# Performance work log

Measured on AMD Instinct MI355X. Metric: run time of the kernel, lower is better.

The kernel has to match this reference:

```python
import jax, jax.numpy as jnp
import numpy as np

N, D = 8192, 128

def setup_inputs() -> dict:
    key = jax.random.key(0)
    kq, kk, kv = jax.random.split(key, 3)
    return {
        "query": jax.random.normal(kq, (N, D), dtype=jnp.float32),
        "key": jax.random.normal(kk, (N, D), dtype=jnp.float32),
        "value": jax.random.normal(kv, (N, D), dtype=jnp.float32),
    }

def reference(query, key, value):
    # FlashAttentionV1 computes exact (non-causal, unmasked) softmax attention:
    # softmax(Q K^T / sqrt(d)) V, via tiled online softmax. The math is
    # identical to the dense formulation below.
    d = query.shape[-1]
    scores = jnp.einsum('qd,kd->qk', query, key) / jnp.sqrt(jnp.asarray(d, query.dtype))
    probs = jax.nn.softmax(scores, axis=-1)
    return jnp.einsum('qk,kd->qd', probs, value)
```

## Files before the change

kernel.cpp:

```cpp
#include <hip/hip_runtime.h>

#define NTOK 8192
#define DH   128
#define QBLK 128
#define KVB  64
#define TILES (NTOK / KVB)

typedef __attribute__((ext_vector_type(8)))  short bf16x8;
typedef __attribute__((ext_vector_type(16))) float f32x16;
typedef __attribute__((ext_vector_type(4)))  unsigned short u16x4;

typedef __attribute__((address_space(1))) const void gv_t;
typedef __attribute__((address_space(3))) void sv_t;

static __device__ __forceinline__ unsigned short f2bf(float x) {
  union { float f; unsigned int u; } a; a.f = x;
  unsigned int r = a.u + 0x7FFFu + ((a.u >> 16) & 1u);
  return (unsigned short)(r >> 16);
}

static __device__ __forceinline__ unsigned pk2(float lo, float hi) {
  unsigned r;
  asm("v_cvt_pk_bf16_f32 %0, %1, %2" : "=v"(r) : "v"(lo), "v"(hi));
  return r;
}

static __device__ __forceinline__ f32x16 zero16() {
  f32x16 v;
  #pragma unroll
  for (int i = 0; i < 16; ++i) v[i] = 0.f;
  return v;
}

__global__ __launch_bounds__(256)
void fa_prep(const float* __restrict__ Kg, const float* __restrict__ Vg,
             char* __restrict__ Kimg, char* __restrict__ Vimg)
{
  const int t = blockIdx.x;
  const int tid = threadIdx.x;

  {
    const int krow = tid >> 2;
    const int kcg  = (tid & 3) * 32;
    const float* src = Kg + ((size_t)t * KVB + krow) * DH + kcg;
    char* drow = Kimg + (size_t)t * 16384 + krow * 256;
    const int sw = (krow & 15) << 4;
    #pragma unroll
    for (int w = 0; w < 4; ++w) {
      float4 a = *reinterpret_cast<const float4*>(src + w * 8);
      float4 b = *reinterpret_cast<const float4*>(src + w * 8 + 4);
      union { bf16x8 v; unsigned short u[8]; } f;
      f.u[0] = f2bf(a.x); f.u[1] = f2bf(a.y); f.u[2] = f2bf(a.z); f.u[3] = f2bf(a.w);
      f.u[4] = f2bf(b.x); f.u[5] = f2bf(b.y); f.u[6] = f2bf(b.z); f.u[7] = f2bf(b.w);
      *reinterpret_cast<bf16x8*>(drow + ((kcg * 2 + w * 16) ^ sw)) = f.v;
    }
  }

  {
    #pragma unroll
    for (int it = 0; it < 2; ++it) {
      int task = tid + it * 256;
      int kvl  = (task & 15) * 4;
      int d0   = (task >> 4) * 4;
      const float* src = Vg + ((size_t)t * KVB + kvl) * DH + d0;
      float4 r0 = *reinterpret_cast<const float4*>(src);
      float4 r1 = *reinterpret_cast<const float4*>(src + DH);
      float4 r2 = *reinterpret_cast<const float4*>(src + 2 * DH);
      float4 r3 = *reinterpret_cast<const float4*>(src + 3 * DH);
      char* base = Vimg + (size_t)t * 16384;
      const int bb = kvl * 2;
      { int d = d0 + 0;
        u16x4 w4 = (u16x4){f2bf(r0.x), f2bf(r1.x), f2bf(r2.x), f2bf(r3.x)};
        *reinterpret_cast<u16x4*>(base + d * 128 + (bb ^ ((d & 15) << 3))) = w4; }
      { int d = d0 + 1;
        u16x4 w4 = (u16x4){f2bf(r0.y), f2bf(r1.y), f2bf(r2.y), f2bf(r3.y)};
        *reinterpret_cast<u16x4*>(base + d * 128 + (bb ^ ((d & 15) << 3))) = w4; }
      { int d = d0 + 2;
        u16x4 w4 = (u16x4){f2bf(r0.z), f2bf(r1.z), f2bf(r2.z), f2bf(r3.z)};
        *reinterpret_cast<u16x4*>(base + d * 128 + (bb ^ ((d & 15) << 3))) = w4; }
      { int d = d0 + 3;
        u16x4 w4 = (u16x4){f2bf(r0.w), f2bf(r1.w), f2bf(r2.w), f2bf(r3.w)};
        *reinterpret_cast<u16x4*>(base + d * 128 + (bb ^ ((d & 15) << 3))) = w4; }
    }
  }
}

static __device__ __forceinline__ void softmax_half(
    const f32x16& st, float& m_run, float& l_run, f32x16* oacc,
    bf16x8& pfa, bf16x8& pfb)
{
  float a0 = fmaxf(st[0],  st[1]),  a1 = fmaxf(st[2],  st[3]);
  float a2 = fmaxf(st[4],  st[5]),  a3 = fmaxf(st[6],  st[7]);
  float a4 = fmaxf(st[8],  st[9]),  a5 = fmaxf(st[10], st[11]);
  float a6 = fmaxf(st[12], st[13]), a7 = fmaxf(st[14], st[15]);
  float b0 = fmaxf(a0, a1), b1 = fmaxf(a2, a3);
  float b2 = fmaxf(a4, a5), b3 = fmaxf(a6, a7);
  float pmax = fmaxf(fmaxf(b0, b1), fmaxf(b2, b3));
  if (!__all(pmax <= m_run + 8.f)) {
    pmax = fmaxf(pmax, __shfl_xor(pmax, 32));
    const float m_new = fmaxf(m_run, pmax);
    const float corr  = (m_run > -1e30f) ? exp2f(m_run - m_new) : 0.f;
    l_run *= corr;
    #pragma unroll
    for (int i = 0; i < 4; ++i) oacc[i] = oacc[i] * corr;
    m_run = m_new;
  }
  float e[16];
  #pragma unroll
  for (int r = 0; r < 16; ++r) e[r] = exp2f(st[r] - m_run);
  float s0 = (e[0] + e[1])   + (e[2] + e[3]);
  float s1 = (e[4] + e[5])   + (e[6] + e[7]);
  float s2 = (e[8] + e[9])   + (e[10] + e[11]);
  float s3 = (e[12] + e[13]) + (e[14] + e[15]);
  l_run += (s0 + s1) + (s2 + s3);
  union { bf16x8 v; unsigned u[4]; } fa, fb;
  fa.u[0] = pk2(e[0],  e[1]);  fa.u[1] = pk2(e[2],  e[3]);
  fa.u[2] = pk2(e[4],  e[5]);  fa.u[3] = pk2(e[6],  e[7]);
  fb.u[0] = pk2(e[8],  e[9]);  fb.u[1] = pk2(e[10], e[11]);
  fb.u[2] = pk2(e[12], e[13]); fb.u[3] = pk2(e[14], e[15]);
  pfa = fa.v; pfb = fb.v;
}

__global__ __launch_bounds__(256, 3)
void fa_fwd(const float* __restrict__ Qg, const char* __restrict__ Kimg,
            const char* __restrict__ Vimg, float* __restrict__ Od,
            float* __restrict__ Mp, float* __restrict__ Lp, int ksplit)
{
  __shared__ __align__(16) char smem[49152];
  const int tid  = threadIdx.x;
  const int lane = tid & 63;
  const int wv   = tid >> 6;
  const int l31  = lane & 31;
  const int hi   = lane >> 5;

  const int q0blk = blockIdx.x * QBLK;
  const int q     = q0blk + wv * 32 + l31;
  const int chunk = blockIdx.y;
  const float QSCALE = 0.1275313310087464f;

  const int bt    = TILES / ksplit;
  const int rem   = TILES - bt * ksplit;
  const int tile0 = chunk * bt + (chunk < rem ? chunk : rem);
  const int nst   = bt + (chunk < rem ? 1 : 0);

  bf16x8 qf[8];
  {
    const float* qs = Qg + (size_t)q * DH + hi * 8;
    #pragma unroll
    for (int kc = 0; kc < 8; ++kc) {
      float4 a = *reinterpret_cast<const float4*>(qs + kc * 16);
      float4 b = *reinterpret_cast<const float4*>(qs + kc * 16 + 4);
      union { bf16x8 v; unsigned u[4]; } f;
      f.u[0] = pk2(a.x * QSCALE, a.y * QSCALE);
      f.u[1] = pk2(a.z * QSCALE, a.w * QSCALE);
      f.u[2] = pk2(b.x * QSCALE, b.y * QSCALE);
      f.u[3] = pk2(b.z * QSCALE, b.w * QSCALE);
      qf[kc] = f.v;
    }
  }

  const char* gbase = (wv < 2 ? Kimg : Vimg);
  const size_t goff = (size_t)(wv & 1) * 8192 + (size_t)lane * 16;
  const int    lK   = (wv & 1) * 8192;
  const int    lV   = 32768 + (wv & 1) * 8192;

#define STAGE_K(B, T) do { if (wv < 2) {                                      \
    const char* _s = gbase + (size_t)(T) * 16384 + goff;                      \
    char* _d = &smem[(B) * 16384 + lK];                                       \
    _Pragma("unroll")                                                         \
    for (int _i = 0; _i < 8; ++_i)                                            \
      __builtin_amdgcn_global_load_lds((gv_t*)(_s + _i * 1024),               \
                                       (sv_t*)(_d + _i * 1024), 16, 0, 0);    \
  } } while (0)

#define STAGE_V(T) do { if (wv >= 2) {                                        \
    const char* _s = gbase + (size_t)(T) * 16384 + goff;                      \
    char* _d = &smem[lV];                                                     \
    _Pragma("unroll")                                                         \
    for (int _i = 0; _i < 8; ++_i)                                            \
      __builtin_amdgcn_global_load_lds((gv_t*)(_s + _i * 1024),               \
                                       (sv_t*)(_d + _i * 1024), 16, 0, 0);    \
  } } while (0)

  STAGE_K(0, tile0);
  STAGE_K(1, tile0 + 1);
  STAGE_V(tile0);

  f32x16 oacc[4];
  #pragma unroll
  for (int i = 0; i < 4; ++i) oacc[i] = zero16();
  float m_run = -INFINITY, l_run = 0.f;

  int cur = 0;
  for (int t = 0; t < nst; ++t) {
    if (wv < 2) {
      if (t + 1 < nst) asm volatile("s_waitcnt vmcnt(8)" ::: "memory");
      else             asm volatile("s_waitcnt vmcnt(0)" ::: "memory");
    }
    __builtin_amdgcn_sched_barrier(0);
    __builtin_amdgcn_s_barrier();

    const char* smK = &smem[cur * 16384];
    const char* smV = &smem[32768];
    const int swk = (l31 & 15) << 4;
    const int swv = (l31 & 15) << 3;

    f32x16 st0 = zero16(), st1 = zero16();
    __builtin_amdgcn_s_setprio(1);
    #pragma unroll
    for (int kc = 0; kc < 8; ++kc) {
      const int cb = (kc * 32 + hi * 16) ^ swk;
      bf16x8 a0 = *reinterpret_cast<const bf16x8*>(smK + l31 * 256 + cb);
      st0 = __builtin_amdgcn_mfma_f32_32x32x16_bf16(a0, qf[kc], st0, 0, 0, 0);
      bf16x8 a1 = *reinterpret_cast<const bf16x8*>(smK + (l31 + 32) * 256 + cb);
      st1 = __builtin_amdgcn_mfma_f32_32x32x16_bf16(a1, qf[kc], st1, 0, 0, 0);
    }
    __builtin_amdgcn_s_setprio(0);

    bf16x8 pf0a, pf0b, pf1a, pf1b;
    softmax_half(st0, m_run, l_run, oacc, pf0a, pf0b);
    softmax_half(st1, m_run, l_run, oacc, pf1a, pf1b);

    if (wv >= 2) asm volatile("s_waitcnt vmcnt(0)" ::: "memory");
    __builtin_amdgcn_sched_barrier(0);
    __builtin_amdgcn_s_barrier();

    __builtin_amdgcn_s_setprio(1);
    #pragma unroll
    for (int c = 0; c < 4; ++c) {
      const bf16x8 pb = (c == 0) ? pf0a : (c == 1) ? pf0b : (c == 2) ? pf1a : pf1b;
      #pragma unroll
      for (int dt = 0; dt < 4; ++dt) {
        const char* vb = smV + (dt * 32 + l31) * 128;
        union { bf16x8 v; u16x4 h[2]; } a;
        a.h[0] = *reinterpret_cast<const u16x4*>(vb + ((c * 32 + 8 * hi) ^ swv));
        a.h[1] = *reinterpret_cast<const u16x4*>(vb + ((c * 32 + 16 + 8 * hi) ^ swv));
        oacc[dt] = __builtin_amdgcn_mfma_f32_32x32x16_bf16(a.v, pb, oacc[dt], 0, 0, 0);
      }
    }
    __builtin_amdgcn_s_setprio(0);

    __builtin_amdgcn_s_barrier();
    if (t + 2 < nst) STAGE_K(cur, tile0 + t + 2);
    if (t + 1 < nst) STAGE_V(tile0 + t + 1);
    cur ^= 1;
  }
#undef STAGE_K
#undef STAGE_V

  const float l_tot = l_run + __shfl_xor(l_run, 32);
  const float scale = (ksplit == 1) ? (1.f / l_tot) : 1.f;
  float* dstB = (ksplit == 1) ? Od : Od + (size_t)chunk * NTOK * DH;

  char* base = &smem[(wv & 1) * 16384];
  const int qloc4 = lane >> 2;
  const int s4    = lane & 3;
  #pragma unroll
  for (int ph = 0; ph < 2; ++ph) {
    __builtin_amdgcn_s_barrier();
    if ((wv >> 1) == ph) {
      #pragma unroll
      for (int dt = 0; dt < 4; ++dt)
        #pragma unroll
        for (int rg = 0; rg < 4; ++rg)
          #pragma unroll
          for (int j = 0; j < 4; ++j) {
            const int d = dt * 32 + rg * 8 + hi * 4 + j;
            *reinterpret_cast<float*>(base + d * 128 + l31 * 4) =
                oacc[dt][rg * 4 + j] * scale;
          }
      asm volatile("s_waitcnt lgkmcnt(0)" ::: "memory");
      __builtin_amdgcn_sched_barrier(0);
      #pragma unroll
      for (int qh = 0; qh < 2; ++qh) {
        const int qloc = qh * 16 + qloc4;
        float* dst = dstB + (size_t)(q0blk + wv * 32 + qloc) * DH;
        #pragma unroll
        for (int i = 0; i < 8; ++i) {
          const int dd = s4 * 4 + i * 16;
          float4 v;
          v.x = *reinterpret_cast<float*>(base + (dd + 0) * 128 + qloc * 4);
          v.y = *reinterpret_cast<float*>(base + (dd + 1) * 128 + qloc * 4);
          v.z = *reinterpret_cast<float*>(base + (dd + 2) * 128 + qloc * 4);
          v.w = *reinterpret_cast<float*>(base + (dd + 3) * 128 + qloc * 4);
          *reinterpret_cast<float4*>(dst + dd) = v;
        }
      }
    }
  }

  if (ksplit > 1 && lane < 32) {
    const int qg = q0blk + wv * 32 + lane;
    Mp[chunk * NTOK + qg] = m_run;
    Lp[chunk * NTOK + qg] = l_tot;
  }
}

__global__ __launch_bounds__(256)
void fa_combine(const float* __restrict__ Op, const float* __restrict__ Mp,
                const float* __restrict__ Lp, float* __restrict__ out, int ksplit)
{
  const int gid = blockIdx.x * 256 + threadIdx.x;
  const int q   = gid >> 5;
  const int dv  = (gid & 31) * 4;
  float mx = -INFINITY;
  for (int c = 0; c < ksplit; ++c) mx = fmaxf(mx, Mp[c * NTOK + q]);
  float den = 0.f;
  float ax = 0.f, ay = 0.f, az = 0.f, aw = 0.f;
  for (int c = 0; c < ksplit; ++c) {
    const float w = exp2f(Mp[c * NTOK + q] - mx);
    den += w * Lp[c * NTOK + q];
    float4 o = *reinterpret_cast<const float4*>(Op + (size_t)c * NTOK * DH + (size_t)q * DH + dv);
    ax += w * o.x; ay += w * o.y; az += w * o.z; aw += w * o.w;
  }
  const float r = 1.f / den;
  float4 res; res.x = ax * r; res.y = ay * r; res.z = az * r; res.w = aw * r;
  *reinterpret_cast<float4*>(out + (size_t)q * DH + dv) = res;
}

extern "C" void kernel_launch(void* const* d_in, const int* in_sizes, int n_in,
                              void* d_out, int out_size, void* d_ws, size_t ws_size,
                              hipStream_t stream)
{
  const float* Q = (const float*)d_in[0];
  const float* K = (const float*)d_in[1];
  const float* V = (const float*)d_in[2];
  float* out = (float*)d_out;

  auto need = [](size_t ks) {
    return ks * (size_t)NTOK * DH * 4 + 2 * ks * (size_t)NTOK * 4;
  };
  int KS = (ws_size >= need(12)) ? 12 : 8;

  char* Kimg = (char*)d_out;
  char* Vimg = Kimg + (size_t)NTOK * 256;

  float* Op = (float*)d_ws;
  float* Mp = Op + (size_t)KS * NTOK * DH;
  float* Lp = Mp + (size_t)KS * NTOK;

  fa_prep<<<TILES, 256, 0, stream>>>(K, V, Kimg, Vimg);
  fa_fwd<<<dim3(NTOK / QBLK, KS), 256, 0, stream>>>(Q, Kimg, Vimg, Op, Mp, Lp, KS);
  fa_combine<<<NTOK * DH / 4 / 256, 256, 0, stream>>>(Op, Mp, Lp, out, KS);
}
```

Before: 73.92 us.

## Software-pipeline QK^T of next tile with PV MFMAs using double-buffered V

Restructures the main attention loop so the QK^T MFMAs for the next KV tile are interleaved with the PV MFMAs of the current tile, and softmax runs on scores computed in the previous iteration. V is now double-buffered in 64KB LDS and K/V prefetches are issued right after softmax. The split count drops from 12 to 8 (or fewer) with occupancy hint lowered to 2 blocks, and the epilogue writes all four waves at once without phasing. This aims to hide softmax and load latency behind matrix work, at the cost of more registers, more LDS and fewer resident blocks.

```diff
diff --git a/kernel.cpp b/kernel.cpp
--- a/kernel.cpp
+++ b/kernel.cpp
@@ -4,7 +4,6 @@
 #define DH   128
 #define QBLK 128
 #define KVB  64
-#define TILES (NTOK / KVB)
 
 typedef __attribute__((ext_vector_type(8)))  short bf16x8;
 typedef __attribute__((ext_vector_type(16))) float f32x16;
@@ -121,12 +120,13 @@
   pfa = fa.v; pfb = fb.v;
 }
 
-__global__ __launch_bounds__(256, 3)
+__global__ __launch_bounds__(256, 2)
 void fa_fwd(const float* __restrict__ Qg, const char* __restrict__ Kimg,
             const char* __restrict__ Vimg, float* __restrict__ Od,
-            float* __restrict__ Mp, float* __restrict__ Lp, int ksplit)
-{
-  __shared__ __align__(16) char smem[49152];
+            float* __restrict__ Mp, float* __restrict__ Lp,
+            int ksplit, int chunk_len)
+{
+  __shared__ __align__(16) char smem[65536];
   const int tid  = threadIdx.x;
   const int lane = tid & 63;
   const int wv   = tid >> 6;
@@ -138,10 +138,8 @@
   const int chunk = blockIdx.y;
   const float QSCALE = 0.1275313310087464f;
 
-  const int bt    = TILES / ksplit;
-  const int rem   = TILES - bt * ksplit;
-  const int tile0 = chunk * bt + (chunk < rem ? chunk : rem);
-  const int nst   = bt + (chunk < rem ? 1 : 0);
+  const int tile0 = (chunk * chunk_len) >> 6;
+  const int nst   = chunk_len >> 6;
 
   bf16x8 qf[8];
   {
@@ -161,21 +159,20 @@
 
   const char* gbase = (wv < 2 ? Kimg : Vimg);
   const size_t goff = (size_t)(wv & 1) * 8192 + (size_t)lane * 16;
-  const int    lK   = (wv & 1) * 8192;
-  const int    lV   = 32768 + (wv & 1) * 8192;
+  const int    lofs = (wv & 1) * 8192;
 
 #define STAGE_K(B, T) do { if (wv < 2) {                                      \
     const char* _s = gbase + (size_t)(T) * 16384 + goff;                      \
-    char* _d = &smem[(B) * 16384 + lK];                                       \
+    char* _d = &smem[(B) * 16384 + lofs];                                     \
     _Pragma("unroll")                                                         \
     for (int _i = 0; _i < 8; ++_i)                                            \
       __builtin_amdgcn_global_load_lds((gv_t*)(_s + _i * 1024),               \
                                        (sv_t*)(_d + _i * 1024), 16, 0, 0);    \
   } } while (0)
 
-#define STAGE_V(T) do { if (wv >= 2) {                                        \
+#define STAGE_V(B, T) do { if (wv >= 2) {                                     \
     const char* _s = gbase + (size_t)(T) * 16384 + goff;                      \
-    char* _d = &smem[lV];                                                     \
+    char* _d = &smem[32768 + (B) * 16384 + lofs];                             \
     _Pragma("unroll")                                                         \
     for (int _i = 0; _i < 8; ++_i)                                            \
       __builtin_amdgcn_global_load_lds((gv_t*)(_s + _i * 1024),               \
@@ -184,29 +181,22 @@
 
   STAGE_K(0, tile0);
   STAGE_K(1, tile0 + 1);
-  STAGE_V(tile0);
+  STAGE_V(0, tile0);
 
   f32x16 oacc[4];
   #pragma unroll
   for (int i = 0; i < 4; ++i) oacc[i] = zero16();
   float m_run = -INFINITY, l_run = 0.f;
-
-  int cur = 0;
-  for (int t = 0; t < nst; ++t) {
-    if (wv < 2) {
-      if (t + 1 < nst) asm volatile("s_waitcnt vmcnt(8)" ::: "memory");
-      else             asm volatile("s_waitcnt vmcnt(0)" ::: "memory");
-    }
-    __builtin_amdgcn_sched_barrier(0);
-    __builtin_amdgcn_s_barrier();
-
-    const char* smK = &smem[cur * 16384];
-    const char* smV = &smem[32768];
-    const int swk = (l31 & 15) << 4;
-    const int swv = (l31 & 15) << 3;
-
-    f32x16 st0 = zero16(), st1 = zero16();
-    __builtin_amdgcn_s_setprio(1);
+  const int swk = (l31 & 15) << 4;
+  const int swv = (l31 & 15) << 3;
+
+  if (wv < 2) asm volatile("s_waitcnt vmcnt(8)" ::: "memory");
+  __builtin_amdgcn_sched_barrier(0);
+  __builtin_amdgcn_s_barrier();
+
+  f32x16 st0 = zero16(), st1 = zero16();
+  {
+    const char* smK = &smem[0];
     #pragma unroll
     for (int kc = 0; kc < 8; ++kc) {
       const int cb = (kc * 32 + hi * 16) ^ swk;
@@ -215,35 +205,59 @@
       bf16x8 a1 = *reinterpret_cast<const bf16x8*>(smK + (l31 + 32) * 256 + cb);
       st1 = __builtin_amdgcn_mfma_f32_32x32x16_bf16(a1, qf[kc], st1, 0, 0, 0);
     }
-    __builtin_amdgcn_s_setprio(0);
-
+  }
+  __builtin_amdgcn_s_barrier();
+
+  for (int t = 0; t < nst; ++t) {
     bf16x8 pf0a, pf0b, pf1a, pf1b;
     softmax_half(st0, m_run, l_run, oacc, pf0a, pf0b);
     softmax_half(st1, m_run, l_run, oacc, pf1a, pf1b);
 
-    if (wv >= 2) asm volatile("s_waitcnt vmcnt(0)" ::: "memory");
+    if (t + 2 < nst) STAGE_K(t & 1, tile0 + t + 2);
+    if (t + 1 < nst) STAGE_V((t + 1) & 1, tile0 + t + 1);
+
+    if (wv < 2) {
+      if (t + 2 < nst) asm volatile("s_waitcnt vmcnt(8)" ::: "memory");
+      else             asm volatile("s_waitcnt vmcnt(0)" ::: "memory");
+    } else {
+      if (t + 1 < nst) asm volatile("s_waitcnt vmcnt(8)" ::: "memory");
+      else             asm volatile("s_waitcnt vmcnt(0)" ::: "memory");
+    }
     __builtin_amdgcn_sched_barrier(0);
     __builtin_amdgcn_s_barrier();
 
+    const char* smK = &smem[((t + 1) & 1) * 16384];
+    const char* smV = &smem[32768 + (t & 1) * 16384];
+    const bool doqk = (t + 1 < nst);
+    f32x16 ns0 = zero16(), ns1 = zero16();
     __builtin_amdgcn_s_setprio(1);
     #pragma unroll
-    for (int c = 0; c < 4; ++c) {
-      const bf16x8 pb = (c == 0) ? pf0a : (c == 1) ? pf0b : (c == 2) ? pf1a : pf1b;
+    for (int g = 0; g < 4; ++g) {
+      if (doqk) {
+        #pragma unroll
+        for (int kk = 0; kk < 2; ++kk) {
+          const int kc = g * 2 + kk;
+          const int cb = (kc * 32 + hi * 16) ^ swk;
+          bf16x8 a0 = *reinterpret_cast<const bf16x8*>(smK + l31 * 256 + cb);
+          ns0 = __builtin_amdgcn_mfma_f32_32x32x16_bf16(a0, qf[kc], ns0, 0, 0, 0);
+          bf16x8 a1 = *reinterpret_cast<const bf16x8*>(smK + (l31 + 32) * 256 + cb);
+          ns1 = __builtin_amdgcn_mfma_f32_32x32x16_bf16(a1, qf[kc], ns1, 0, 0, 0);
+        }
+      }
+      const bf16x8 pb = (g == 0) ? pf0a : (g == 1) ? pf0b : (g == 2) ? pf1a : pf1b;
       #pragma unroll
       for (int dt = 0; dt < 4; ++dt) {
         const char* vb = smV + (dt * 32 + l31) * 128;
         union { bf16x8 v; u16x4 h[2]; } a;
-        a.h[0] = *reinterpret_cast<const u16x4*>(vb + ((c * 32 + 8 * hi) ^ swv));
-        a.h[1] = *reinterpret_cast<const u16x4*>(vb + ((c * 32 + 16 + 8 * hi) ^ swv));
+        a.h[0] = *reinterpret_cast<const u16x4*>(vb + ((g * 32 + 8 * hi) ^ swv));
+        a.h[1] = *reinterpret_cast<const u16x4*>(vb + ((g * 32 + 16 + 8 * hi) ^ swv));
         oacc[dt] = __builtin_amdgcn_mfma_f32_32x32x16_bf16(a.v, pb, oacc[dt], 0, 0, 0);
       }
     }
     __builtin_amdgcn_s_setprio(0);
+    st0 = ns0; st1 = ns1;
 
     __builtin_amdgcn_s_barrier();
-    if (t + 2 < nst) STAGE_K(cur, tile0 + t + 2);
-    if (t + 1 < nst) STAGE_V(tile0 + t + 1);
-    cur ^= 1;
   }
 #undef STAGE_K
 #undef STAGE_V
@@ -252,40 +266,34 @@
   const float scale = (ksplit == 1) ? (1.f / l_tot) : 1.f;
   float* dstB = (ksplit == 1) ? Od : Od + (size_t)chunk * NTOK * DH;
 
-  char* base = &smem[(wv & 1) * 16384];
+  char* base = &smem[0] + wv * 16384;
+  #pragma unroll
+  for (int dt = 0; dt < 4; ++dt)
+    #pragma unroll
+    for (int rg = 0; rg < 4; ++rg)
+      #pragma unroll
+      for (int j = 0; j < 4; ++j) {
+        const int d = dt * 32 + rg * 8 + hi * 4 + j;
+        *reinterpret_cast<float*>(base + d * 128 + l31 * 4) =
+            oacc[dt][rg * 4 + j] * scale;
+      }
+  asm volatile("s_waitcnt lgkmcnt(0)" ::: "memory");
+  __builtin_amdgcn_sched_barrier(0);
   const int qloc4 = lane >> 2;
   const int s4    = lane & 3;
   #pragma unroll
-  for (int ph = 0; ph < 2; ++ph) {
-    __builtin_amdgcn_s_barrier();
-    if ((wv >> 1) == ph) {
-      #pragma unroll
-      for (int dt = 0; dt < 4; ++dt)
-        #pragma unroll
-        for (int rg = 0; rg < 4; ++rg)
-          #pragma unroll
-          for (int j = 0; j < 4; ++j) {
-            const int d = dt * 32 + rg * 8 + hi * 4 + j;
-            *reinterpret_cast<float*>(base + d * 128 + l31 * 4) =
-                oacc[dt][rg * 4 + j] * scale;
-          }
-      asm volatile("s_waitcnt lgkmcnt(0)" ::: "memory");
-      __builtin_amdgcn_sched_barrier(0);
-      #pragma unroll
-      for (int qh = 0; qh < 2; ++qh) {
-        const int qloc = qh * 16 + qloc4;
-        float* dst = dstB + (size_t)(q0blk + wv * 32 + qloc) * DH;
-        #pragma unroll
-        for (int i = 0; i < 8; ++i) {
-          const int dd = s4 * 4 + i * 16;
-          float4 v;
-          v.x = *reinterpret_cast<float*>(base + (dd + 0) * 128 + qloc * 4);
-          v.y = *reinterpret_cast<float*>(base + (dd + 1) * 128 + qloc * 4);
-          v.z = *reinterpret_cast<float*>(base + (dd + 2) * 128 + qloc * 4);
-          v.w = *reinterpret_cast<float*>(base + (dd + 3) * 128 + qloc * 4);
-          *reinterpret_cast<float4*>(dst + dd) = v;
-        }
-      }
+  for (int qh = 0; qh < 2; ++qh) {
+    const int qloc = qh * 16 + qloc4;
+    float* dst = dstB + (size_t)(q0blk + wv * 32 + qloc) * DH;
+    #pragma unroll
+    for (int i = 0; i < 8; ++i) {
+      const int dd = s4 * 4 + i * 16;
+      float4 v;
+      v.x = *reinterpret_cast<float*>(base + (dd + 0) * 128 + qloc * 4);
+      v.y = *reinterpret_cast<float*>(base + (dd + 1) * 128 + qloc * 4);
+      v.z = *reinterpret_cast<float*>(base + (dd + 2) * 128 + qloc * 4);
+      v.w = *reinterpret_cast<float*>(base + (dd + 3) * 128 + qloc * 4);
+      *reinterpret_cast<float4*>(dst + dd) = v;
     }
   }
 
@@ -330,7 +338,7 @@
   auto need = [](size_t ks) {
     return ks * (size_t)NTOK * DH * 4 + 2 * ks * (size_t)NTOK * 4;
   };
-  int KS = (ws_size >= need(12)) ? 12 : 8;
+  int KS = (ws_size >= need(8)) ? 8 : (ws_size >= need(4)) ? 4 : 2;
 
   char* Kimg = (char*)d_out;
   char* Vimg = Kimg + (size_t)NTOK * 256;
@@ -339,7 +347,8 @@
   float* Mp = Op + (size_t)KS * NTOK * DH;
   float* Lp = Mp + (size_t)KS * NTOK;
 
-  fa_prep<<<TILES, 256, 0, stream>>>(K, V, Kimg, Vimg);
-  fa_fwd<<<dim3(NTOK / QBLK, KS), 256, 0, stream>>>(Q, Kimg, Vimg, Op, Mp, Lp, KS);
+  fa_prep<<<NTOK / KVB, 256, 0, stream>>>(K, V, Kimg, Vimg);
+  fa_fwd<<<dim3(NTOK / QBLK, KS), 256, 0, stream>>>(Q, Kimg, Vimg, Op, Mp, Lp,
+                                                    KS, NTOK / KS);
   fa_combine<<<NTOK * DH / 4 / 256, 256, 0, stream>>>(Op, Mp, Lp, out, KS);
 }
```

Measured after the change: 69.54 us. 1.06x faster.
